# Performance work log

Hardware: AMD Instinct MI355X
Metric: run time of the kernel (lower is better)

## Reference

```python
import jax, jax.numpy as jnp
import numpy as np

L = 4          # GAT_LAYERS
HEADS = 4      # N_HEADS
H = 64         # transformer hidden dim
DH = H // HEADS
FIN = 32       # NODE_EMBED_SIZE
A = 15         # gats.num_actions (readout size)
OBS = 1500     # flattened obs dim
HS = 512       # hidden_size (policy FC)
NOUT = 15      # num_outputs
VH = 128       # VALUE_HIDDENS
B = 128        # batch of graphs
N = 1000       # nodes per map graph
TOT = B * N
DEG = 4
E = TOT * DEG


def _lin(key, fan_in, shape):
    return jax.random.normal(key, shape, jnp.float32) * (1.0 / np.sqrt(fan_in))


def setup_inputs() -> dict:
    key = jax.random.key(0)
    ks = jax.random.split(key, 30)
    node_feats = jax.random.normal(ks[0], (TOT, FIN), jnp.float32)
    obs = jax.random.normal(ks[1], (B, OBS), jnp.float32)
    # batched-graph edges: endpoints stay within each graph (DGL batch semantics)
    off = (jnp.arange(B) * N)[:, None]
    edge_src = (jax.random.randint(ks[2], (B, N * DEG), 0, N) + off).reshape(-1).astype(jnp.int32)
    edge_dst = (jax.random.randint(ks[3], (B, N * DEG), 0, N) + off).reshape(-1).astype(jnp.int32)
    agent_nodes = (jax.random.randint(ks[4], (B,), 0, N) + jnp.arange(B) * N).astype(jnp.int32)
    p = {
        'W_in': _lin(ks[5], FIN, (FIN, H)),
        'Wq': _lin(ks[6], H, (L, H, H)), 'Wk': _lin(ks[7], H, (L, H, H)),
        'Wv': _lin(ks[8], H, (L, H, H)), 'Wo': _lin(ks[9], H, (L, H, H)),
        'ln1_g': jnp.ones((L, H), jnp.float32), 'ln1_b': jnp.zeros((L, H), jnp.float32),
        'W1': _lin(ks[10], H, (L, H, 2 * H)), 'b1': jnp.zeros((L, 2 * H), jnp.float32),
        'W2': _lin(ks[11], 2 * H, (L, 2 * H, H)), 'b2': jnp.zeros((L, H), jnp.float32),
        'ln2_g': jnp.ones((L, H), jnp.float32), 'ln2_b': jnp.zeros((L, H), jnp.float32),
        'Wr': _lin(ks[12], H, (H, A)), 'br': jnp.zeros((A,), jnp.float32),
        'Wp1': _lin(ks[13], A + OBS, (A + OBS, HS)), 'bp1': jnp.zeros((HS,), jnp.float32),
        'Wp2': _lin(ks[14], HS, (HS, HS)), 'bp2': jnp.zeros((HS,), jnp.float32),
        'Wlog': _lin(ks[15], HS, (HS, NOUT)), 'blog': jnp.zeros((NOUT,), jnp.float32),
        'Wv1': _lin(ks[16], OBS, (OBS, VH)), 'bv1': jnp.zeros((VH,), jnp.float32),
        'Wv2': _lin(ks[17], VH, (VH, VH)), 'bv2': jnp.zeros((VH,), jnp.float32),
        'Wvo': _lin(ks[18], VH, (VH, 1)), 'bvo': jnp.zeros((1,), jnp.float32),
    }
    return dict(node_feats=node_feats, obs=obs, edge_src=edge_src, edge_dst=edge_dst,
                agent_nodes=agent_nodes, **p)


def _layernorm(x, g, b):
    m = x.mean(-1, keepdims=True)
    v = ((x - m) ** 2).mean(-1, keepdims=True)
    return (x - m) * jax.lax.rsqrt(v + 1e-5) * g + b


def reference(node_feats, obs, edge_src, edge_dst, agent_nodes, W_in, Wq, Wk, Wv, Wo,
              ln1_g, ln1_b, W1, b1, W2, b2, ln2_g, ln2_b, Wr, br,
              Wp1, bp1, Wp2, bp2, Wlog, blog, Wv1, bv1, Wv2, bv2, Wvo, bvo):
    n = node_feats.shape[0]
    x = node_feats @ W_in                                   # [n, H]
    inv_sqrt_dh = np.float32(1.0 / np.sqrt(DH))
    for l in range(L):
        q = (x @ Wq[l]).reshape(n, HEADS, DH)
        k = (x @ Wk[l]).reshape(n, HEADS, DH)
        v = (x @ Wv[l]).reshape(n, HEADS, DH)
        # per-edge attention scores, softmax over incoming edges of each dst node
        s = jnp.sum(q[edge_dst] * k[edge_src], axis=-1) * inv_sqrt_dh   # [E, HEADS]
        m = jax.ops.segment_max(s, edge_dst, num_segments=n)            # [n, HEADS]
        w = jnp.exp(s - m[edge_dst])
        denom = jax.ops.segment_sum(w, edge_dst, num_segments=n)        # [n, HEADS]
        agg = jax.ops.segment_sum(w[:, :, None] * v[edge_src], edge_dst, num_segments=n)
        attn = (agg / (denom[:, :, None] + 1e-9)).reshape(n, H) @ Wo[l]
        x = _layernorm(x + attn, ln1_g[l], ln1_b[l])
        h = jax.nn.relu(x @ W1[l] + b1[l]) @ W2[l] + b2[l]
        x = _layernorm(x + h, ln2_g[l], ln2_b[l])
    gat_out = x[agent_nodes] @ Wr + br                      # [B, A] per-agent action features
    feat = jnp.tanh(jnp.concatenate([gat_out, obs], axis=1) @ Wp1 + bp1)
    feat = jnp.tanh(feat @ Wp2 + bp2)
    logits = feat @ Wlog + blog                             # [B, NOUT]
    vh = jnp.tanh(obs @ Wv1 + bv1)
    vh = jnp.tanh(vh @ Wv2 + bv2)
    value = (vh @ Wvo + bvo)[:, 0]                          # [B]
    return logits, value
```

## Files before the change

### kernel.cpp

```cpp
#include <hip/hip_runtime.h>
#include <hip/hip_bf16.h>
#include <cstdint>
#include <cstddef>

#define DEV static __device__ __forceinline__

constexpr int GRAPHS = 128;
constexpr int NPG    = 1000;
constexpr int EPG    = 4000;
constexpr int TOTN   = GRAPHS * NPG;
constexpr int TOTE   = GRAPHS * EPG;
constexpr int HD     = 64;
constexpr int OBSD   = 1500;
constexpr int AD     = 15;

typedef __attribute__((ext_vector_type(8))) short bf16x8;
typedef __attribute__((ext_vector_type(4))) float f32x4;

DEV unsigned short f2b(float f){
  unsigned u = __float_as_uint(f);
  return (unsigned short)((u + 0x7fffu + ((u >> 16) & 1u)) >> 16);
}
DEV float b2f(unsigned short s){ return __uint_as_float((unsigned)s << 16); }

DEV void fma4(float4& a, float s, const float4 w){
  a.x = fmaf(s, w.x, a.x); a.y = fmaf(s, w.y, a.y);
  a.z = fmaf(s, w.z, a.z); a.w = fmaf(s, w.w, a.w);
}

DEV ushort4 pack4(float4 v){
  ushort4 r; r.x=f2b(v.x); r.y=f2b(v.y); r.z=f2b(v.z); r.w=f2b(v.w); return r;
}

__global__ __launch_bounds__(256) void k_wprep(const float* __restrict__ Wq,
    const float* __restrict__ Wk, const float* __restrict__ Wv,
    const float* __restrict__ Wo, const float* __restrict__ W1,
    const float* __restrict__ W2, unsigned short* __restrict__ wpack){
  int e = blockIdx.x*256 + threadIdx.x;
  int l = e >> 15;
  int r = e & 32767;
  float val;
  if (r < 12288){
    int c = r >> 6, k = r & 63;
    val = (c < 64)  ? Wq[l*4096 + k*64 + c]
        : (c < 128) ? Wk[l*4096 + k*64 + (c-64)]
                    : Wv[l*4096 + k*64 + (c-128)];
  } else if (r < 16384){
    int i = r - 12288; int c = i >> 6, k = i & 63;
    val = Wo[l*4096 + k*64 + c];
  } else if (r < 24576){
    int i = r - 16384; int c = i >> 6, k = i & 63;
    val = W1[l*8192 + k*128 + c];
  } else {
    int i = r - 24576; int c = i >> 7, k = i & 127;
    val = W2[l*8192 + k*64 + c];
  }
  wpack[e] = f2b(val);
}

__global__ __launch_bounds__(256) void k_zero(int* __restrict__ cnt){
  cnt[blockIdx.x*256 + threadIdx.x] = 0;
}

__global__ __launch_bounds__(256) void k_hist(const int* __restrict__ edst,
                                              int* __restrict__ cnt){
  int e = blockIdx.x*256 + threadIdx.x;
  atomicAdd(&cnt[edst[e]], 1);
}

__global__ __launch_bounds__(1024) void k_scan(const int* __restrict__ cnt,
    int* __restrict__ rstart, int* __restrict__ cursor){
  __shared__ int s[1024];
  const int g = blockIdx.x, tid = threadIdx.x;
  int v = (tid < NPG) ? cnt[g*NPG + tid] : 0;
  s[tid] = v;
  __syncthreads();
  #pragma unroll
  for (int off=1; off<1024; off<<=1){
    int t = (tid >= off) ? s[tid-off] : 0;
    __syncthreads();
    s[tid] += t;
    __syncthreads();
  }
  if (tid < NPG){
    int r = g*EPG + (s[tid] - v);
    rstart[g*NPG+tid] = r;
    cursor[g*NPG+tid] = r;
  }
}

__global__ __launch_bounds__(256) void k_scatter(const int* __restrict__ esrc,
    const int* __restrict__ edst, int* __restrict__ cursor,
    int* __restrict__ esorted){
  int e = blockIdx.x*256 + threadIdx.x;
  int pos = atomicAdd(&cursor[edst[e]], 1);
  esorted[pos] = esrc[e];
}

__global__ __launch_bounds__(256) void k_in(const float* __restrict__ nf,
                                            const float* __restrict__ Win,
                                            unsigned short* __restrict__ xb){
  __shared__ float  s_nf[256*36];
  __shared__ float4 s_w[512];
  const int tid = threadIdx.x;
  const int node0 = blockIdx.x * 256;
  const float4* W4 = (const float4*)Win;
  s_w[tid] = W4[tid]; s_w[tid+256] = W4[tid+256];
  const float4* nf4 = (const float4*)nf;
  float4* snf4 = (float4*)s_nf;
  #pragma unroll
  for (int r=0;r<8;r++){
    int i = tid + 256*r; int n = i>>3, k4 = i&7;
    snf4[n*9 + k4] = nf4[(size_t)(node0+n)*8 + k4];
  }
  __syncthreads();
  const int ng = tid>>2, cg = tid&3;
  float4 acc[4][4];
  #pragma unroll
  for (int i=0;i<4;i++){ acc[i][0]=make_float4(0,0,0,0); acc[i][1]=make_float4(0,0,0,0);
                         acc[i][2]=make_float4(0,0,0,0); acc[i][3]=make_float4(0,0,0,0); }
  #pragma unroll 4
  for (int k=0;k<32;k++){
    float nv[4];
    #pragma unroll
    for (int i=0;i<4;i++) nv[i] = s_nf[(ng + 64*i)*36 + k];
    float4 w[4];
    #pragma unroll
    for (int j=0;j<4;j++) w[j] = s_w[k*16 + cg*4 + j];
    #pragma unroll
    for (int i=0;i<4;i++){
      #pragma unroll
      for (int j=0;j<4;j++) fma4(acc[i][j], nv[i], w[j]);
    }
  }
  ushort4* xb4 = (ushort4*)xb;
  #pragma unroll
  for (int i=0;i<4;i++){
    size_t nidx = (size_t)(node0 + ng + 64*i) * 16;
    #pragma unroll
    for (int j=0;j<4;j++) xb4[nidx + cg*4 + j] = pack4(acc[i][j]);
  }
}

__global__ __launch_bounds__(256) void k_qkv_m(const unsigned short* __restrict__ xb,
    const unsigned short* __restrict__ wqkvT,
    unsigned short* __restrict__ qkv){
  __shared__ short s_w[192*72];
  __shared__ short s_st[4][16*104];
  const int tid = threadIdx.x;
  const int node0 = blockIdx.x * 256;
  {
    const unsigned* src = (const unsigned*)wqkvT;
    unsigned* dst = (unsigned*)s_w;
    #pragma unroll
    for (int r=0;r<24;r++){
      int j = tid + 256*r;
      int c = j >> 5, kk = j & 31;
      dst[c*36 + kk] = src[j];
    }
  }
  __syncthreads();
  const int lane = tid & 63, wave = tid >> 6;
  const int m = lane & 15, quad = lane >> 4;
  const int rowbase = node0 + wave*64;
  bf16x8 af[4][2];
  #pragma unroll
  for (int rt=0;rt<4;rt++){
    const unsigned short* xp = xb + (size_t)(rowbase + rt*16 + m)*64 + quad*8;
    af[rt][0] = *(const bf16x8*)xp;
    af[rt][1] = *(const bf16x8*)(xp + 32);
  }
  short* st = s_st[wave];
  #pragma unroll
  for (int rt=0;rt<4;rt++){
    #pragma unroll
    for (int half=0; half<2; half++){
      #pragma unroll
      for (int c6=0;c6<6;c6++){
        int ct = half*6 + c6;
        bf16x8 b0 = *(const bf16x8*)&s_w[(ct*16+m)*72 + quad*8];
        bf16x8 b1 = *(const bf16x8*)&s_w[(ct*16+m)*72 + 32 + quad*8];
        f32x4 acc = {0.f,0.f,0.f,0.f};
        acc = __builtin_amdgcn_mfma_f32_16x16x32_bf16(af[rt][0], b0, acc, 0,0,0);
        acc = __builtin_amdgcn_mfma_f32_16x16x32_bf16(af[rt][1], b1, acc, 0,0,0);
        #pragma unroll
        for (int i=0;i<4;i++)
          st[(quad*4+i)*104 + c6*16 + m] = (short)f2b(acc[i]);
      }
      #pragma unroll
      for (int j=0;j<3;j++){
        int flat = (j*64 + lane)*8;
        int r = flat / 96, c = flat % 96;
        bf16x8 v = *(const bf16x8*)&st[r*104 + c];
        *(bf16x8*)(qkv + (size_t)(rowbase + rt*16 + r)*192 + half*96 + c) = v;
      }
    }
  }
}

__global__ __launch_bounds__(256) void k_edge2(const unsigned short* __restrict__ qkv,
    const int* __restrict__ rstart, const int* __restrict__ cnt,
    const int* __restrict__ esorted, unsigned short* __restrict__ attn_in){
  const int tid = threadIdx.x;
  const int wb = (blockIdx.x & 7)*1000 + (blockIdx.x >> 3);
  const int lane = tid & 63;
  const int sub  = lane >> 4;
  const int dg   = lane & 15;
  const int wave = tid >> 6;
  const int node = wb*16 + wave*4 + sub;
  const ushort4* row = (const ushort4*)(qkv + (size_t)node*192);
  ushort4 qu = row[dg];
  float q0 = b2f(qu.x), q1 = b2f(qu.y), q2 = b2f(qu.z), q3 = b2f(qu.w);
  const int rs = rstart[node];
  const int n  = cnt[node];
  float a0=0.f, a1=0.f, a2=0.f, a3=0.f, den=0.f;
  for (int i=0;i<n;i++){
    int src = esorted[rs + i];
    ushort4 ku = *(const ushort4*)(qkv + (size_t)src*192 + 64 + dg*4);
    ushort4 vu = *(const ushort4*)(qkv + (size_t)src*192 + 128 + dg*4);
    float p = q0*b2f(ku.x) + q1*b2f(ku.y) + q2*b2f(ku.z) + q3*b2f(ku.w);
    p += __shfl_xor(p, 1);
    p += __shfl_xor(p, 2);
    float w = __expf(p * 0.25f);
    den += w;
    a0 = fmaf(w, b2f(vu.x), a0);
    a1 = fmaf(w, b2f(vu.y), a1);
    a2 = fmaf(w, b2f(vu.z), a2);
    a3 = fmaf(w, b2f(vu.w), a3);
  }
  float inv = 1.0f/(den + 1e-9f);
  ushort4 o;
  o.x = f2b(a0*inv); o.y = f2b(a1*inv); o.z = f2b(a2*inv); o.w = f2b(a3*inv);
  ((ushort4*)attn_in)[(size_t)node*16 + dg] = o;
}

__global__ __launch_bounds__(256) void k_attn_m(const unsigned short* __restrict__ attn_in,
    const unsigned short* __restrict__ woT, const float* __restrict__ lg,
    const float* __restrict__ lb, unsigned short* __restrict__ xb){
  __shared__ short s_w[64*72];
  __shared__ short s_st[4][16*72];
  const int tid = threadIdx.x;
  const int node0 = blockIdx.x*256;
  {
    const unsigned* src = (const unsigned*)woT;
    unsigned* dst = (unsigned*)s_w;
    #pragma unroll
    for (int r=0;r<8;r++){
      int j = tid + 256*r;
      int c = j >> 5, kk = j & 31;
      dst[c*36 + kk] = src[j];
    }
  }
  __syncthreads();
  const int lane = tid&63, wave = tid>>6;
  const int m = lane&15, quad = lane>>4;
  const int rowbase = node0 + wave*64;
  bf16x8 bf[4][2];
  #pragma unroll
  for (int ct=0;ct<4;ct++){
    bf[ct][0] = *(const bf16x8*)&s_w[(ct*16+m)*72 + quad*8];
    bf[ct][1] = *(const bf16x8*)&s_w[(ct*16+m)*72 + 32 + quad*8];
  }
  float g[4], bb[4];
  #pragma unroll
  for (int ct=0;ct<4;ct++){ g[ct]=lg[ct*16+m]; bb[ct]=lb[ct*16+m]; }
  short* st = s_st[wave];
  #pragma unroll
  for (int rt=0;rt<4;rt++){
    const unsigned short* ap = attn_in + (size_t)(rowbase + rt*16 + m)*64 + quad*8;
    bf16x8 a0 = *(const bf16x8*)ap;
    bf16x8 a1 = *(const bf16x8*)(ap + 32);
    f32x4 acc[4];
    #pragma unroll
    for (int ct=0;ct<4;ct++){
      f32x4 z = {0.f,0.f,0.f,0.f};
      z = __builtin_amdgcn_mfma_f32_16x16x32_bf16(a0, bf[ct][0], z, 0,0,0);
      z = __builtin_amdgcn_mfma_f32_16x16x32_bf16(a1, bf[ct][1], z, 0,0,0);
      acc[ct] = z;
    }
    #pragma unroll
    for (int i=0;i<4;i++){
      size_t row = (size_t)(rowbase + rt*16 + quad*4 + i)*64;
      float v0 = acc[0][i] + b2f(xb[row + m]);
      float v1 = acc[1][i] + b2f(xb[row + 16 + m]);
      float v2 = acc[2][i] + b2f(xb[row + 32 + m]);
      float v3 = acc[3][i] + b2f(xb[row + 48 + m]);
      float sm = v0+v1+v2+v3;
      float sq = v0*v0+v1*v1+v2*v2+v3*v3;
      #pragma unroll
      for (int mk=1; mk<16; mk<<=1){ sm += __shfl_xor(sm, mk); sq += __shfl_xor(sq, mk); }
      float mean = sm*0.015625f;
      float var  = sq*0.015625f - mean*mean;
      float rs   = rsqrtf(var + 1e-5f);
      int rl = quad*4 + i;
      st[rl*72 + m]      = (short)f2b((v0-mean)*rs*g[0]+bb[0]);
      st[rl*72 + 16 + m] = (short)f2b((v1-mean)*rs*g[1]+bb[1]);
      st[rl*72 + 32 + m] = (short)f2b((v2-mean)*rs*g[2]+bb[2]);
      st[rl*72 + 48 + m] = (short)f2b((v3-mean)*rs*g[3]+bb[3]);
    }
    #pragma unroll
    for (int j=0;j<2;j++){
      int flat = (j*64 + lane)*8;
      int r = flat >> 6, c = flat & 63;
      bf16x8 v = *(const bf16x8*)&st[r*72 + c];
      *(bf16x8*)(xb + (size_t)(rowbase + rt*16 + r)*64 + c) = v;
    }
  }
}

__global__ __launch_bounds__(256) void k_ffn_m(unsigned short* __restrict__ xb,
    const unsigned short* __restrict__ w1T, const float* __restrict__ b1_l,
    const unsigned short* __restrict__ w2T, const float* __restrict__ b2_l,
    const float* __restrict__ lg, const float* __restrict__ lb){
  __shared__ short s_w1[128*72];
  __shared__ short s_w2[64*136];
  __shared__ short s_st[4][16*136];
  const int tid = threadIdx.x;
  const int node0 = blockIdx.x*256;
  {
    const unsigned* src = (const unsigned*)w1T;
    unsigned* dst = (unsigned*)s_w1;
    #pragma unroll
    for (int r=0;r<16;r++){
      int j = tid + 256*r;
      int c = j >> 5, kk = j & 31;
      dst[c*36 + kk] = src[j];
    }
  }
  {
    const unsigned* src = (const unsigned*)w2T;
    unsigned* dst = (unsigned*)s_w2;
    #pragma unroll
    for (int r=0;r<16;r++){
      int j = tid + 256*r;
      int c = j >> 6, kk = j & 63;
      dst[c*68 + kk] = src[j];
    }
  }
  __syncthreads();
  const int lane = tid&63, wave = tid>>6;
  const int m = lane&15, quad = lane>>4;
  const int rowbase = node0 + wave*64;
  bf16x8 af[4][2];
  #pragma unroll
  for (int rt=0;rt<4;rt++){
    const unsigned short* xp = xb + (size_t)(rowbase + rt*16 + m)*64 + quad*8;
    af[rt][0] = *(const bf16x8*)xp;
    af[rt][1] = *(const bf16x8*)(xp + 32);
  }
  float g[4], bb[4], b2v[4];
  #pragma unroll
  for (int ct=0;ct<4;ct++){ g[ct]=lg[ct*16+m]; bb[ct]=lb[ct*16+m]; b2v[ct]=b2_l[ct*16+m]; }
  short* st = s_st[wave];
  #pragma unroll
  for (int rt=0;rt<4;rt++){
    #pragma unroll
    for (int ct=0;ct<8;ct++){
      bf16x8 b0 = *(const bf16x8*)&s_w1[(ct*16+m)*72 + quad*8];
      bf16x8 b1 = *(const bf16x8*)&s_w1[(ct*16+m)*72 + 32 + quad*8];
      float bias = b1_l[ct*16+m];
      f32x4 acc = {0.f,0.f,0.f,0.f};
      acc = __builtin_amdgcn_mfma_f32_16x16x32_bf16(af[rt][0], b0, acc, 0,0,0);
      acc = __builtin_amdgcn_mfma_f32_16x16x32_bf16(af[rt][1], b1, acc, 0,0,0);
      #pragma unroll
      for (int i=0;i<4;i++)
        st[(quad*4+i)*136 + ct*16 + m] = (short)f2b(fmaxf(acc[i]+bias, 0.f));
    }
    bf16x8 h0 = *(const bf16x8*)&st[m*136 + quad*8];
    bf16x8 h1 = *(const bf16x8*)&st[m*136 + 32 + quad*8];
    bf16x8 h2 = *(const bf16x8*)&st[m*136 + 64 + quad*8];
    bf16x8 h3 = *(const bf16x8*)&st[m*136 + 96 + quad*8];
    f32x4 acc2[4];
    #pragma unroll
    for (int ct=0;ct<4;ct++){
      f32x4 z = {0.f,0.f,0.f,0.f};
      z = __builtin_amdgcn_mfma_f32_16x16x32_bf16(h0, *(const bf16x8*)&s_w2[(ct*16+m)*136 + quad*8],      z, 0,0,0);
      z = __builtin_amdgcn_mfma_f32_16x16x32_bf16(h1, *(const bf16x8*)&s_w2[(ct*16+m)*136 + 32 + quad*8], z, 0,0,0);
      z = __builtin_amdgcn_mfma_f32_16x16x32_bf16(h2, *(const bf16x8*)&s_w2[(ct*16+m)*136 + 64 + quad*8], z, 0,0,0);
      z = __builtin_amdgcn_mfma_f32_16x16x32_bf16(h3, *(const bf16x8*)&s_w2[(ct*16+m)*136 + 96 + quad*8], z, 0,0,0);
      acc2[ct] = z;
    }
    #pragma unroll
    for (int i=0;i<4;i++){
      size_t row = (size_t)(rowbase + rt*16 + quad*4 + i)*64;
      float v0 = acc2[0][i] + b2v[0] + b2f(xb[row + m]);
      float v1 = acc2[1][i] + b2v[1] + b2f(xb[row + 16 + m]);
      float v2 = acc2[2][i] + b2v[2] + b2f(xb[row + 32 + m]);
      float v3 = acc2[3][i] + b2v[3] + b2f(xb[row + 48 + m]);
      float sm = v0+v1+v2+v3;
      float sq = v0*v0+v1*v1+v2*v2+v3*v3;
      #pragma unroll
      for (int mk=1; mk<16; mk<<=1){ sm += __shfl_xor(sm, mk); sq += __shfl_xor(sq, mk); }
      float mean = sm*0.015625f;
      float var  = sq*0.015625f - mean*mean;
      float rs   = rsqrtf(var + 1e-5f);
      int rl = quad*4 + i;
      st[rl*136 + m]      = (short)f2b((v0-mean)*rs*g[0]+bb[0]);
      st[rl*136 + 16 + m] = (short)f2b((v1-mean)*rs*g[1]+bb[1]);
      st[rl*136 + 32 + m] = (short)f2b((v2-mean)*rs*g[2]+bb[2]);
      st[rl*136 + 48 + m] = (short)f2b((v3-mean)*rs*g[3]+bb[3]);
    }
    #pragma unroll
    for (int j=0;j<2;j++){
      int flat = (j*64 + lane)*8;
      int r = flat >> 6, c = flat & 63;
      bf16x8 v = *(const bf16x8*)&st[r*136 + c];
      *(bf16x8*)(xb + (size_t)(rowbase + rt*16 + r)*64 + c) = v;
    }
  }
}

__global__ __launch_bounds__(256) void k_feat(const unsigned short* __restrict__ xb,
    const float* __restrict__ obs, const int* __restrict__ agents,
    const float* __restrict__ Wr, const float* __restrict__ br,
    float* __restrict__ feat){
  __shared__ float s_xa[64];
  const int b = blockIdx.x, tid = threadIdx.x;
  if (tid < 64) s_xa[tid] = b2f(xb[(size_t)agents[b]*HD + tid]);
  __syncthreads();
  if (tid < AD){
    float a = br[tid];
    #pragma unroll 8
    for (int k=0;k<HD;k++) a = fmaf(s_xa[k], Wr[k*AD + tid], a);
    feat[(size_t)b*1536 + tid] = a;
  }
  for (int i=tid;i<OBSD;i+=256) feat[(size_t)b*1536 + AD + i] = obs[(size_t)b*OBSD + i];
  if (tid < 21) feat[(size_t)b*1536 + 1515 + tid] = 0.f;
}

template<int ROWS, int COLS, int CH, int KS, int N>
__global__ __launch_bounds__(ROWS*COLS) void k_gemm_part(
    const float* __restrict__ A, int lda, int K,
    const float* __restrict__ W, float* __restrict__ part){
  constexpr int BT = ROWS*COLS;
  __shared__ float s_a[ROWS*CH];
  const int tid = threadIdx.x;
  const int ct = blockIdx.x, rg = blockIdx.y, ks = blockIdx.z;
  const int chunk = (K + KS - 1) / KS;
  const int k0 = ks * chunk;
  const int len = min(K - k0, chunk);
  const int row0 = rg * ROWS;
  #pragma unroll
  for (int rr=0; rr<ROWS; rr++)
    for (int i=tid; i<len; i+=BT)
      s_a[rr*CH + i] = A[(size_t)(row0+rr)*lda + k0 + i];
  __syncthreads();
  const int r = tid / COLS, c = tid % COLS;
  const float* wp = W + (size_t)k0*N + ct*COLS + c;
  const float* ap = s_a + r*CH;
  float acc = 0.f;
  #pragma unroll 8
  for (int k=0;k<len;k++) acc = fmaf(ap[k], wp[(size_t)k*N], acc);
  part[((size_t)ks*128 + row0 + r)*N + ct*COLS + c] = acc;
}

template<int KS, int N, bool TANH>
__global__ __launch_bounds__(256) void k_reduce(const float* __restrict__ part,
    const float* __restrict__ bias, float* __restrict__ out, int MN){
  const int idx = blockIdx.x*256 + threadIdx.x;
  if (idx >= MN) return;
  float s = bias[idx & (N-1)];
  #pragma unroll
  for (int ks=0;ks<KS;ks++) s += part[(size_t)ks*MN + idx];
  out[idx] = TANH ? tanhf(s) : s;
}

__global__ __launch_bounds__(256) void k_logits(const float* __restrict__ f2,
    const float* __restrict__ Wlog, const float* __restrict__ blog,
    float* __restrict__ out){
  __shared__ float s_f[512];
  __shared__ float s_p[16*AD];
  const int b = blockIdx.x, tid = threadIdx.x;
  s_f[tid]     = f2[(size_t)b*512 + tid];
  s_f[tid+256] = f2[(size_t)b*512 + 256 + tid];
  __syncthreads();
  if (tid < 240){
    int c = tid % AD, kc = tid / AD;
    float a = 0.f;
    #pragma unroll 8
    for (int j=0;j<32;j++){ int k = kc*32 + j; a = fmaf(s_f[k], Wlog[k*AD + c], a); }
    s_p[tid] = a;
  }
  __syncthreads();
  if (tid < AD){
    float a = blog[tid];
    #pragma unroll
    for (int kc=0;kc<16;kc++) a += s_p[kc*AD + tid];
    out[(size_t)b*AD + tid] = a;
  }
}

__global__ __launch_bounds__(128) void k_vfin(const float* __restrict__ vh,
    const float* __restrict__ Wv2, const float* __restrict__ bv2,
    const float* __restrict__ Wvo, const float* __restrict__ bvo,
    float* __restrict__ out){
  __shared__ float s_v[128];
  __shared__ float s_r[128];
  const int b = blockIdx.x, tid = threadIdx.x;
  s_v[tid] = vh[(size_t)b*128 + tid];
  __syncthreads();
  float a = bv2[tid];
  #pragma unroll 8
  for (int k=0;k<128;k++) a = fmaf(s_v[k], Wv2[k*128 + tid], a);
  s_r[tid] = tanhf(a) * Wvo[tid];
  __syncthreads();
  if (tid < 64){
    float v = s_r[tid] + s_r[tid+64];
    #pragma unroll
    for (int m=32;m>=1;m>>=1) v += __shfl_xor(v, m);
    if (tid==0) out[GRAPHS*AD + b] = v + bvo[0];
  }
}

extern "C" void kernel_launch(void* const* d_in, const int* in_sizes, int n_in,
                              void* d_out, int out_size, void* d_ws, size_t ws_size,
                              hipStream_t stream) {
  (void)in_sizes; (void)n_in; (void)out_size; (void)ws_size;
  const float* nf     = (const float*)d_in[0];
  const float* obs    = (const float*)d_in[1];
  const int*   esrc   = (const int*)d_in[2];
  const int*   edst   = (const int*)d_in[3];
  const int*   agents = (const int*)d_in[4];
  const float* Win    = (const float*)d_in[5];
  const float* Wq     = (const float*)d_in[6];
  const float* Wk     = (const float*)d_in[7];
  const float* Wv     = (const float*)d_in[8];
  const float* Wo     = (const float*)d_in[9];
  const float* ln1g   = (const float*)d_in[10];
  const float* ln1b   = (const float*)d_in[11];
  const float* W1     = (const float*)d_in[12];
  const float* b1     = (const float*)d_in[13];
  const float* W2     = (const float*)d_in[14];
  const float* b2     = (const float*)d_in[15];
  const float* ln2g   = (const float*)d_in[16];
  const float* ln2b   = (const float*)d_in[17];
  const float* Wr     = (const float*)d_in[18];
  const float* br     = (const float*)d_in[19];
  const float* Wp1    = (const float*)d_in[20];
  const float* bp1    = (const float*)d_in[21];
  const float* Wp2    = (const float*)d_in[22];
  const float* bp2    = (const float*)d_in[23];
  const float* Wlog   = (const float*)d_in[24];
  const float* blog   = (const float*)d_in[25];
  const float* Wv1    = (const float*)d_in[26];
  const float* bv1    = (const float*)d_in[27];
  const float* Wv2    = (const float*)d_in[28];
  const float* bv2    = (const float*)d_in[29];
  const float* Wvo    = (const float*)d_in[30];
  const float* bvo    = (const float*)d_in[31];
  float* out = (float*)d_out;

  unsigned short* xb      = (unsigned short*)d_ws;
  unsigned short* qkv     = xb + (size_t)TOTN*HD;
  unsigned short* attn_in = qkv + (size_t)TOTN*192;
  unsigned short* wpack   = attn_in + (size_t)TOTN*HD;
  int* cnt     = (int*)(wpack + 131072);
  int* rstart  = cnt + TOTN;
  int* cursor  = rstart + TOTN;
  int* esorted = cursor + TOTN;
  float* feat = (float*)(esorted + TOTE);
  float* f1   = feat + 128*1536;
  float* f2   = f1 + 128*512;
  float* vh   = f2 + 128*512;
  float* part = vh + 128*128;

  k_wprep  <<<512, 256, 0, stream>>>(Wq, Wk, Wv, Wo, W1, W2, wpack);
  k_zero   <<<TOTN/256, 256, 0, stream>>>(cnt);
  k_hist   <<<TOTE/256, 256, 0, stream>>>(edst, cnt);
  k_scan   <<<GRAPHS, 1024, 0, stream>>>(cnt, rstart, cursor);
  k_scatter<<<TOTE/256, 256, 0, stream>>>(esrc, edst, cursor, esorted);

  k_in<<<TOTN/256, 256, 0, stream>>>(nf, Win, xb);
  for (int l=0; l<4; l++){
    const unsigned short* wl = wpack + l*32768;
    k_qkv_m <<<TOTN/256, 256, 0, stream>>>(xb, wl, qkv);
    k_edge2 <<<TOTN/16, 256, 0, stream>>>(qkv, rstart, cnt, esorted, attn_in);
    k_attn_m<<<TOTN/256, 256, 0, stream>>>(attn_in, wl + 12288,
                                           ln1g + l*64, ln1b + l*64, xb);
    k_ffn_m <<<TOTN/256, 256, 0, stream>>>(xb, wl + 16384, b1 + l*128,
                                           wl + 24576, b2 + l*64,
                                           ln2g + l*64, ln2b + l*64);
  }
  k_feat<<<GRAPHS, 256, 0, stream>>>(xb, obs, agents, Wr, br, feat);
  k_gemm_part<2,256,384,4,512><<<dim3(2,64,4), 512, 0, stream>>>(feat, 1536, 1515, Wp1, part);
  k_reduce<4,512,true><<<256, 256, 0, stream>>>(part, bp1, f1, 128*512);
  k_gemm_part<2,256,256,2,512><<<dim3(2,64,2), 512, 0, stream>>>(f1, 512, 512, Wp2, part);
  k_reduce<2,512,true><<<256, 256, 0, stream>>>(part, bp2, f2, 128*512);
  k_logits<<<GRAPHS, 256, 0, stream>>>(f2, Wlog, blog, out);
  k_gemm_part<4,128,192,8,128><<<dim3(1,32,8), 512, 0, stream>>>(obs, 1500, 1500, Wv1, part);
  k_reduce<8,128,true><<<64, 256, 0, stream>>>(part, bv1, vh, 128*128);
  k_vfin<<<GRAPHS, 128, 0, stream>>>(vh, Wv2, bv2, Wvo, bvo, out);
}
```

Before: 534.5 us.

## Prefetch next edge in attention loop and fuse head GEMM reductions

The edge aggregation loop now issues the loads for the next neighbor's K/V rows before computing the current one, to hide gather latency. The FFN kernel hoists its per-column bias loads out of the inner loop. The policy and value heads fold the feature concat, split-K reductions, bias and tanh into the consuming kernels, which removes the k_feat and k_reduce launches and their intermediate buffers. The tail kernels are small next to the four-layer graph loop, so most of any change should come from the edge prefetch, which costs extra registers and a branch.

Measured after the change: 519.9 us. -2.7%, faster.

```diff
diff --git a/kernel.cpp b/kernel.cpp
--- a/kernel.cpp
+++ b/kernel.cpp
@@ -214,19 +214,25 @@
   const int rs = rstart[node];
   const int n  = cnt[node];
   float a0=0.f, a1=0.f, a2=0.f, a3=0.f, den=0.f;
+  int src = (n > 0) ? esorted[rs] : 0;
+  ushort4 ku = *(const ushort4*)(qkv + (size_t)src*192 + 64 + dg*4);
+  ushort4 vu = *(const ushort4*)(qkv + (size_t)src*192 + 128 + dg*4);
   for (int i=0;i<n;i++){
-    int src = esorted[rs + i];
-    ushort4 ku = *(const ushort4*)(qkv + (size_t)src*192 + 64 + dg*4);
-    ushort4 vu = *(const ushort4*)(qkv + (size_t)src*192 + 128 + dg*4);
-    float p = q0*b2f(ku.x) + q1*b2f(ku.y) + q2*b2f(ku.z) + q3*b2f(ku.w);
+    ushort4 cku = ku, cvu = vu;
+    if (i+1 < n){
+      int s2 = esorted[rs + i + 1];
+      ku = *(const ushort4*)(qkv + (size_t)s2*192 + 64 + dg*4);
+      vu = *(const ushort4*)(qkv + (size_t)s2*192 + 128 + dg*4);
+    }
+    float p = q0*b2f(cku.x) + q1*b2f(cku.y) + q2*b2f(cku.z) + q3*b2f(cku.w);
     p += __shfl_xor(p, 1);
     p += __shfl_xor(p, 2);
     float w = __expf(p * 0.25f);
     den += w;
-    a0 = fmaf(w, b2f(vu.x), a0);
-    a1 = fmaf(w, b2f(vu.y), a1);
-    a2 = fmaf(w, b2f(vu.z), a2);
-    a3 = fmaf(w, b2f(vu.w), a3);
+    a0 = fmaf(w, b2f(cvu.x), a0);
+    a1 = fmaf(w, b2f(cvu.y), a1);
+    a2 = fmaf(w, b2f(cvu.z), a2);
+    a3 = fmaf(w, b2f(cvu.w), a3);
   }
   float inv = 1.0f/(den + 1e-9f);
   ushort4 o;
@@ -351,6 +357,9 @@
   float g[4], bb[4], b2v[4];
   #pragma unroll
   for (int ct=0;ct<4;ct++){ g[ct]=lg[ct*16+m]; bb[ct]=lb[ct*16+m]; b2v[ct]=b2_l[ct*16+m]; }
+  float b1v[8];
+  #pragma unroll
+  for (int ct=0;ct<8;ct++) b1v[ct]=b1_l[ct*16+m];
   short* st = s_st[wave];
   #pragma unroll
   for (int rt=0;rt<4;rt++){
@@ -358,13 +367,12 @@
     for (int ct=0;ct<8;ct++){
       bf16x8 b0 = *(const bf16x8*)&s_w1[(ct*16+m)*72 + quad*8];
       bf16x8 b1 = *(const bf16x8*)&s_w1[(ct*16+m)*72 + 32 + quad*8];
-      float bias = b1_l[ct*16+m];
       f32x4 acc = {0.f,0.f,0.f,0.f};
       acc = __builtin_amdgcn_mfma_f32_16x16x32_bf16(af[rt][0], b0, acc, 0,0,0);
       acc = __builtin_amdgcn_mfma_f32_16x16x32_bf16(af[rt][1], b1, acc, 0,0,0);
       #pragma unroll
       for (int i=0;i<4;i++)
-        st[(quad*4+i)*136 + ct*16 + m] = (short)f2b(fmaxf(acc[i]+bias, 0.f));
+        st[(quad*4+i)*136 + ct*16 + m] = (short)f2b(fmaxf(acc[i]+b1v[ct], 0.f));
     }
     bf16x8 h0 = *(const bf16x8*)&st[m*136 + quad*8];
     bf16x8 h1 = *(const bf16x8*)&st[m*136 + 32 + quad*8];
@@ -410,22 +418,96 @@
   }
 }
 
-__global__ __launch_bounds__(256) void k_feat(const unsigned short* __restrict__ xb,
+__global__ __launch_bounds__(512) void k_fc1(const unsigned short* __restrict__ xb,
     const float* __restrict__ obs, const int* __restrict__ agents,
     const float* __restrict__ Wr, const float* __restrict__ br,
-    float* __restrict__ feat){
-  __shared__ float s_xa[64];
+    const float* __restrict__ Wp1, float* __restrict__ part1){
+  constexpr int ROWS=2, COLS=256, CH=384, K=1515, N=512;
+  const int chunk = 379;
+  __shared__ float s_a[ROWS*CH];
+  const int tid = threadIdx.x;
+  const int ct = blockIdx.x, rg = blockIdx.y, ks = blockIdx.z;
+  const int k0 = ks * chunk;
+  const int len = min(K - k0, chunk);
+  const int row0 = rg * ROWS;
+  #pragma unroll
+  for (int rr=0; rr<ROWS; rr++)
+    for (int i=tid; i<len; i+=512){
+      int k = k0 + i;
+      if (k >= AD) s_a[rr*CH + i] = obs[(size_t)(row0+rr)*OBSD + (k-AD)];
+    }
+  if (ks==0 && tid < ROWS*AD){
+    int rr = tid/AD, c = tid%AD;
+    int b = row0 + rr;
+    const unsigned short* xa = xb + (size_t)agents[b]*HD;
+    float a = br[c];
+    #pragma unroll 8
+    for (int k=0;k<HD;k++) a = fmaf(b2f(xa[k]), Wr[k*AD + c], a);
+    s_a[rr*CH + c] = a;
+  }
+  __syncthreads();
+  const int r = tid / COLS, c = tid % COLS;
+  const float* wp = Wp1 + (size_t)k0*N + ct*COLS + c;
+  const float* ap = s_a + r*CH;
+  float acc = 0.f;
+  #pragma unroll 8
+  for (int k=0;k<len;k++) acc = fmaf(ap[k], wp[(size_t)k*N], acc);
+  part1[((size_t)ks*128 + row0 + r)*N + ct*COLS + c] = acc;
+}
+
+__global__ __launch_bounds__(512) void k_fc2(const float* __restrict__ part1,
+    const float* __restrict__ bp1, const float* __restrict__ Wp2,
+    float* __restrict__ part2){
+  constexpr int ROWS=2, COLS=256, CH=256, N=512;
+  __shared__ float s_a[ROWS*CH];
+  const int tid = threadIdx.x;
+  const int ct = blockIdx.x, rg = blockIdx.y, ks = blockIdx.z;
+  const int k0 = ks * CH;
+  const int row0 = rg * ROWS;
+  #pragma unroll
+  for (int rr=0; rr<ROWS; rr++)
+    for (int i=tid; i<CH; i+=512){
+      int k = k0 + i;
+      float s = bp1[k];
+      #pragma unroll
+      for (int j=0;j<4;j++) s += part1[((size_t)j*128 + row0+rr)*512 + k];
+      s_a[rr*CH + i] = tanhf(s);
+    }
+  __syncthreads();
+  const int r = tid / COLS, c = tid % COLS;
+  const float* wp = Wp2 + (size_t)k0*N + ct*COLS + c;
+  const float* ap = s_a + r*CH;
+  float acc = 0.f;
+  #pragma unroll 8
+  for (int k=0;k<CH;k++) acc = fmaf(ap[k], wp[(size_t)k*N], acc);
+  part2[((size_t)ks*128 + row0 + r)*N + ct*COLS + c] = acc;
+}
+
+__global__ __launch_bounds__(256) void k_logits(const float* __restrict__ part2,
+    const float* __restrict__ bp2, const float* __restrict__ Wlog,
+    const float* __restrict__ blog, float* __restrict__ out){
+  __shared__ float s_f[512];
+  __shared__ float s_p[16*AD];
   const int b = blockIdx.x, tid = threadIdx.x;
-  if (tid < 64) s_xa[tid] = b2f(xb[(size_t)agents[b]*HD + tid]);
+  for (int i=tid;i<512;i+=256){
+    float s = bp2[i] + part2[(size_t)b*512 + i] + part2[(size_t)(128+b)*512 + i];
+    s_f[i] = tanhf(s);
+  }
+  __syncthreads();
+  if (tid < 240){
+    int c = tid % AD, kc = tid / AD;
+    float a = 0.f;
+    #pragma unroll 8
+    for (int j=0;j<32;j++){ int k = kc*32 + j; a = fmaf(s_f[k], Wlog[k*AD + c], a); }
+    s_p[tid] = a;
+  }
   __syncthreads();
   if (tid < AD){
-    float a = br[tid];
-    #pragma unroll 8
-    for (int k=0;k<HD;k++) a = fmaf(s_xa[k], Wr[k*AD + tid], a);
-    feat[(size_t)b*1536 + tid] = a;
-  }
-  for (int i=tid;i<OBSD;i+=256) feat[(size_t)b*1536 + AD + i] = obs[(size_t)b*OBSD + i];
-  if (tid < 21) feat[(size_t)b*1536 + 1515 + tid] = 0.f;
+    float a = blog[tid];
+    #pragma unroll
+    for (int kc=0;kc<16;kc++) a += s_p[kc*AD + tid];
+    out[(size_t)b*AD + tid] = a;
+  }
 }
 
 template<int ROWS, int COLS, int CH, int KS, int N>
@@ -454,50 +536,19 @@
   part[((size_t)ks*128 + row0 + r)*N + ct*COLS + c] = acc;
 }
 
-template<int KS, int N, bool TANH>
-__global__ __launch_bounds__(256) void k_reduce(const float* __restrict__ part,
-    const float* __restrict__ bias, float* __restrict__ out, int MN){
-  const int idx = blockIdx.x*256 + threadIdx.x;
-  if (idx >= MN) return;
-  float s = bias[idx & (N-1)];
-  #pragma unroll
-  for (int ks=0;ks<KS;ks++) s += part[(size_t)ks*MN + idx];
-  out[idx] = TANH ? tanhf(s) : s;
-}
-
-__global__ __launch_bounds__(256) void k_logits(const float* __restrict__ f2,
-    const float* __restrict__ Wlog, const float* __restrict__ blog,
-    float* __restrict__ out){
-  __shared__ float s_f[512];
-  __shared__ float s_p[16*AD];
-  const int b = blockIdx.x, tid = threadIdx.x;
-  s_f[tid]     = f2[(size_t)b*512 + tid];
-  s_f[tid+256] = f2[(size_t)b*512 + 256 + tid];
-  __syncthreads();
-  if (tid < 240){
-    int c = tid % AD, kc = tid / AD;
-    float a = 0.f;
-    #pragma unroll 8
-    for (int j=0;j<32;j++){ int k = kc*32 + j; a = fmaf(s_f[k], Wlog[k*AD + c], a); }
-    s_p[tid] = a;
-  }
-  __syncthreads();
-  if (tid < AD){
-    float a = blog[tid];
-    #pragma unroll
-    for (int kc=0;kc<16;kc++) a += s_p[kc*AD + tid];
-    out[(size_t)b*AD + tid] = a;
-  }
-}
-
-__global__ __launch_bounds__(128) void k_vfin(const float* __restrict__ vh,
-    const float* __restrict__ Wv2, const float* __restrict__ bv2,
-    const float* __restrict__ Wvo, const float* __restrict__ bvo,
-    float* __restrict__ out){
+__global__ __launch_bounds__(128) void k_vfin(const float* __restrict__ partv,
+    const float* __restrict__ bv1, const float* __restrict__ Wv2,
+    const float* __restrict__ bv2, const float* __restrict__ Wvo,
+    const float* __restrict__ bvo, float* __restrict__ out){
   __shared__ float s_v[128];
   __shared__ float s_r[128];
   const int b = blockIdx.x, tid = threadIdx.x;
-  s_v[tid] = vh[(size_t)b*128 + tid];
+  {
+    float s = bv1[tid];
+    #pragma unroll
+    for (int j=0;j<8;j++) s += partv[((size_t)j*128 + b)*128 + tid];
+    s_v[tid] = tanhf(s);
+  }
   __syncthreads();
   float a = bv2[tid];
   #pragma unroll 8
@@ -558,11 +609,9 @@
   int* rstart  = cnt + TOTN;
   int* cursor  = rstart + TOTN;
   int* esorted = cursor + TOTN;
-  float* feat = (float*)(esorted + TOTE);
-  float* f1   = feat + 128*1536;
-  float* f2   = f1 + 128*512;
-  float* vh   = f2 + 128*512;
-  float* part = vh + 128*128;
+  float* part1 = (float*)(esorted + TOTE);
+  float* part2 = part1 + 4*128*512;
+  float* partv = part2 + 2*128*512;
 
   k_wprep  <<<512, 256, 0, stream>>>(Wq, Wk, Wv, Wo, W1, W2, wpack);
   k_zero   <<<TOTN/256, 256, 0, stream>>>(cnt);
@@ -581,13 +630,9 @@
                                            wl + 24576, b2 + l*64,
                                            ln2g + l*64, ln2b + l*64);
   }
-  k_feat<<<GRAPHS, 256, 0, stream>>>(xb, obs, agents, Wr, br, feat);
-  k_gemm_part<2,256,384,4,512><<<dim3(2,64,4), 512, 0, stream>>>(feat, 1536, 1515, Wp1, part);
-  k_reduce<4,512,true><<<256, 256, 0, stream>>>(part, bp1, f1, 128*512);
-  k_gemm_part<2,256,256,2,512><<<dim3(2,64,2), 512, 0, stream>>>(f1, 512, 512, Wp2, part);
-  k_reduce<2,512,true><<<256, 256, 0, stream>>>(part, bp2, f2, 128*512);
-  k_logits<<<GRAPHS, 256, 0, stream>>>(f2, Wlog, blog, out);
-  k_gemm_part<4,128,192,8,128><<<dim3(1,32,8), 512, 0, stream>>>(obs, 1500, 1500, Wv1, part);
-  k_reduce<8,128,true><<<64, 256, 0, stream>>>(part, bv1, vh, 128*128);
-  k_vfin<<<GRAPHS, 128, 0, stream>>>(vh, Wv2, bv2, Wvo, bvo, out);
-}
+  k_fc1   <<<dim3(2,64,4), 512, 0, stream>>>(xb, obs, agents, Wr, br, Wp1, part1);
+  k_fc2   <<<dim3(2,64,2), 512, 0, stream>>>(part1, bp1, Wp2, part2);
+  k_logits<<<GRAPHS, 256, 0, stream>>>(part2, bp2, Wlog, blog, out);
+  k_gemm_part<4,128,192,8,128><<<dim3(1,32,8), 512, 0, stream>>>(obs, 1500, 1500, Wv1, partv);
+  k_vfin  <<<GRAPHS, 128, 0, stream>>>(partv, bv1, Wv2, bv2, Wvo, bvo, out);
+}
```
